# Performance work log

Hardware: AMD Instinct MI355X
Metric: run time of the kernel (lower is better)

## Reference

```python
import jax, jax.numpy as jnp
import numpy as np

PI_APPROX = 3.1415926  # the source uses 3.1415926, not math.pi
N_RINGS = 10
N_ANGLES = 36  # k in range(0, 360, 10)


def setup_inputs() -> dict:
    key = jax.random.key(0)
    k1, k2, k3 = jax.random.split(key, 3)
    B, N = 32, 16384
    pred = jax.random.normal(k1, (B, N_RINGS), dtype=jnp.float32)
    target = jax.random.normal(k2, (B, N, 3), dtype=jnp.float32)
    trans_feat = jax.random.normal(k3, (B, 256), dtype=jnp.float32)
    return {"pred": pred, "target": target, "trans_feat": trans_feat}


def _generate_points(pred):
    # pred: [B, 10] radii. For ring j: center = [0.04, 0.15*j - 0.7, 0.0],
    # axis = y, firstPoint (centered) = [-r, 0, 0]. Rotating about y by angle a:
    # R @ [-r,0,0] = [-r*cos(a), 0, r*sin(a)]; then add center back.
    B = pred.shape[0]
    j = jnp.arange(N_RINGS, dtype=pred.dtype)
    cy = 0.15 * j - 0.7                                   # [10]
    ang = jnp.arange(0, 360, 10, dtype=pred.dtype) * (2.0 * PI_APPROX / 360.0)  # [36]
    c, s = jnp.cos(ang), jnp.sin(ang)
    r = pred[:, :, None]                                  # [B,10,1]
    px = -r * c[None, None, :] + 0.04                     # [B,10,36]
    py = jnp.broadcast_to(cy[None, :, None], px.shape)    # [B,10,36]
    pz = r * s[None, None, :]                             # [B,10,36]
    pts = jnp.stack([px, py, pz], axis=-1)                # [B,10,36,3]
    return pts.reshape(B, N_RINGS * N_ANGLES, 3)          # [B,360,3]


def reference(pred, target, trans_feat):
    B = pred.shape[0]
    pts = _generate_points(pred.reshape(B, N_RINGS))      # [B,360,3]
    # squared pairwise distances via ||a||^2 + ||b||^2 - 2 a.b
    d2 = (jnp.sum(pts * pts, axis=-1)[:, :, None]
          + jnp.sum(target * target, axis=-1)[:, None, :]
          - 2.0 * jnp.einsum('bpd,bnd->bpn', pts, target))  # [B,360,N]
    d2 = jnp.maximum(d2, 0.0)
    # original: min over target of ||pt - tgt||, then squared == min of squared dist
    min_d2 = jnp.min(d2, axis=-1)                         # [B,360]
    return jnp.mean(min_d2)
```

## Files before the change

### kernel.cpp

```cpp
#include <hip/hip_runtime.h>
#include <math.h>
#include <float.h>

#define N_RINGS  10
#define N_ANGLES 36
#define NP       (N_RINGS * N_ANGLES)
#define PI_APPROX 3.1415926f

#define BLOCK  256
#define WPB    4
#define CHUNK  512
#define NPAIR  (CHUNK / 2)
#define PPT    6

typedef float f2 __attribute__((ext_vector_type(2)));

__global__ __launch_bounds__(BLOCK, 4) void chamfer_minbuf(
    const float* __restrict__ pred,
    const float* __restrict__ target,
    unsigned int* __restrict__ minbuf,
    int N, int chunks)
{
    __shared__ float4 txy[NPAIR];
    __shared__ float4 tzw[NPAIR];
    __shared__ float  pm[WPB * NP];
    __shared__ float  cs_c[N_ANGLES], cs_s[N_ANGLES];

    const int b   = blockIdx.x / chunks;
    const int cg  = blockIdx.x % chunks;
    const int n0  = cg * CHUNK;
    const int tid = threadIdx.x;
    const int cnt = min(CHUNK, N - n0);
    const int npairs = (cnt + 1) >> 1;

    if (tid < N_ANGLES) {
        float angf = (float)(10 * tid) * (2.0f * PI_APPROX / 360.0f);
        double ang = (double)angf;
        cs_c[tid] = (float)cos(ang);
        cs_s[tid] = (float)sin(ang);
    }
    for (int p = tid; p < npairs; p += BLOCK) {
        const int i0 = 2 * p;
        const int i1 = min(2 * p + 1, cnt - 1);
        const float* t0 = target + ((size_t)b * N + (size_t)(n0 + i0)) * 3;
        const float* t1 = target + ((size_t)b * N + (size_t)(n0 + i1)) * 3;
        float x0 = t0[0], y0 = t0[1], z0 = t0[2];
        float x1 = t1[0], y1 = t1[1], z1 = t1[2];
        float w0 = x0 * x0 + y0 * y0 + z0 * z0;
        float w1 = x1 * x1 + y1 * y1 + z1 * z1;
        txy[p] = make_float4(x0, x1, y0, y1);
        tzw[p] = make_float4(z0, z1, w0, w1);
    }
    __syncthreads();

    const int lane = tid & 63;
    const int w    = tid >> 6;

    f2 qx2[PPT], qy2[PPT], qz2[PPT];
    float m[PPT], pp2[PPT];
    #pragma unroll
    for (int k = 0; k < PPT; ++k) {
        int s = lane + 64 * k;
        int j = s / N_ANGLES;
        int a = s - j * N_ANGLES;
        int jc = (j < N_RINGS) ? j : (N_RINGS - 1);
        float r  = pred[b * N_RINGS + jc];
        float px = -r * cs_c[a] + 0.04f;
        float py = 0.15f * (float)jc - 0.7f;
        float pz = r * cs_s[a];
        pp2[k] = px * px + py * py + pz * pz;
        float qxv = -2.0f * px, qyv = -2.0f * py, qzv = -2.0f * pz;
        qx2[k] = (f2){qxv, qxv};
        qy2[k] = (f2){qyv, qyv};
        qz2[k] = (f2){qzv, qzv};
        m[k]   = FLT_MAX;
    }

    #pragma unroll 4
    for (int k = w; k < npairs; k += WPB) {
        float4 A  = txy[k];
        float4 Bz = tzw[k];
        f2 X  = {A.x,  A.y };
        f2 Y  = {A.z,  A.w };
        f2 Z  = {Bz.x, Bz.y};
        f2 W2 = {Bz.z, Bz.w};
        #pragma unroll
        for (int i = 0; i < PPT; ++i) {
            f2 h = __builtin_elementwise_fma(qz2[i], Z, W2);
            h = __builtin_elementwise_fma(qy2[i], Y, h);
            h = __builtin_elementwise_fma(qx2[i], X, h);
            m[i] = fminf(fminf(m[i], h.x), h.y);
        }
    }

    #pragma unroll
    for (int k = 0; k < PPT; ++k) {
        int s = lane + 64 * k;
        if (s < NP) pm[w * NP + s] = fmaxf(pp2[k] + m[k], 0.0f);
    }
    __syncthreads();

    for (int p = tid; p < NP; p += BLOCK) {
        float v = fminf(fminf(pm[p], pm[NP + p]),
                        fminf(pm[2 * NP + p], pm[3 * NP + p]));
        atomicMin(&minbuf[b * NP + p], __float_as_uint(v));
    }
}

__global__ __launch_bounds__(1024) void reduce_mean(
    const unsigned int* __restrict__ minbuf, float* __restrict__ out,
    int count)
{
    __shared__ double sm[16];
    const int tid = threadIdx.x;
    double s = 0.0;
    const int n4 = count >> 2;
    const uint4* v4 = (const uint4*)minbuf;
    for (int i = tid; i < n4; i += 1024) {
        uint4 u = v4[i];
        s += (double)__uint_as_float(u.x) + (double)__uint_as_float(u.y)
           + (double)__uint_as_float(u.z) + (double)__uint_as_float(u.w);
    }
    for (int i = 4 * n4 + tid; i < count; i += 1024)
        s += (double)__uint_as_float(minbuf[i]);
    #pragma unroll
    for (int off = 32; off > 0; off >>= 1)
        s += __shfl_down(s, off, 64);
    if ((tid & 63) == 0) sm[tid >> 6] = s;
    __syncthreads();
    if (tid == 0) {
        double tot = 0.0;
        for (int wv = 0; wv < 16; ++wv) tot += sm[wv];
        out[0] = (float)(tot / (double)count);
    }
}

extern "C" void kernel_launch(void* const* d_in, const int* in_sizes, int n_in,
                              void* d_out, int out_size, void* d_ws, size_t ws_size,
                              hipStream_t stream) {
    const float* pred   = (const float*)d_in[0];
    const float* target = (const float*)d_in[1];

    const int B = in_sizes[0] / N_RINGS;
    const int N = in_sizes[1] / (3 * B);
    const int chunks = (N + CHUNK - 1) / CHUNK;
    const int count  = B * NP;

    unsigned int* minbuf = (unsigned int*)d_ws;
    float* out = (float*)d_out;

    hipMemsetAsync(minbuf, 0xFF, (size_t)count * sizeof(unsigned int), stream);

    hipLaunchKernelGGL(chamfer_minbuf, dim3(B * chunks), dim3(BLOCK), 0, stream,
                       pred, target, minbuf, N, chunks);
    hipLaunchKernelGGL(reduce_mean, dim3(1), dim3(1024), 0, stream,
                       minbuf, out, count);
}
```

Baseline: 81.48 us.

## Replace atomicMin and memset with per-chunk partials and multi-block reduction

The main kernel now writes per-chunk minimum values to a partial buffer instead of doing global atomicMin into a memset-initialized buffer. This removes the memset launch and the atomic contention. A new multi-block reduce kernel takes the min across chunks for each point, sums the results, and uses an atomic counter so the last block computes the final mean. The cost is a larger workspace (B*chunks*360 floats) and the reduction having to read all partials.

Result: slower. 91.19 us (+11.9%).

```diff
diff --git a/kernel.cpp b/kernel.cpp
--- a/kernel.cpp
+++ b/kernel.cpp
@@ -12,13 +12,15 @@
 #define CHUNK  512
 #define NPAIR  (CHUNK / 2)
 #define PPT    6
+#define RBLOCK 256
 
 typedef float f2 __attribute__((ext_vector_type(2)));
 
-__global__ __launch_bounds__(BLOCK, 4) void chamfer_minbuf(
+__global__ __launch_bounds__(BLOCK, 4) void chamfer_partial(
     const float* __restrict__ pred,
     const float* __restrict__ target,
-    unsigned int* __restrict__ minbuf,
+    float* __restrict__ partial,
+    unsigned int* __restrict__ counter,
     int N, int chunks)
 {
     __shared__ float4 txy[NPAIR];
@@ -32,6 +34,9 @@
     const int tid = threadIdx.x;
     const int cnt = min(CHUNK, N - n0);
     const int npairs = (cnt + 1) >> 1;
+
+    if (blockIdx.x == 0 && tid == 0)
+        *counter = 0u;
 
     if (tid < N_ANGLES) {
         float angf = (float)(10 * tid) * (2.0f * PI_APPROX / 360.0f);
@@ -100,38 +105,58 @@
     }
     __syncthreads();
 
+    float* dst = partial + ((size_t)b * chunks + cg) * NP;
     for (int p = tid; p < NP; p += BLOCK) {
         float v = fminf(fminf(pm[p], pm[NP + p]),
                         fminf(pm[2 * NP + p], pm[3 * NP + p]));
-        atomicMin(&minbuf[b * NP + p], __float_as_uint(v));
+        dst[p] = v;
     }
 }
 
-__global__ __launch_bounds__(1024) void reduce_mean(
-    const unsigned int* __restrict__ minbuf, float* __restrict__ out,
-    int count)
+__global__ __launch_bounds__(RBLOCK) void reduce_minmean(
+    const float* __restrict__ partial,
+    double* __restrict__ sums,
+    unsigned int* __restrict__ counter,
+    float* __restrict__ out,
+    int chunks, int count, int nblocks)
 {
-    __shared__ double sm[16];
+    __shared__ double sm[RBLOCK / 64];
     const int tid = threadIdx.x;
+    const int gid = blockIdx.x * RBLOCK + tid;
+    const int lane = tid & 63;
+    const int w    = tid >> 6;
+
     double s = 0.0;
-    const int n4 = count >> 2;
-    const uint4* v4 = (const uint4*)minbuf;
-    for (int i = tid; i < n4; i += 1024) {
-        uint4 u = v4[i];
-        s += (double)__uint_as_float(u.x) + (double)__uint_as_float(u.y)
-           + (double)__uint_as_float(u.z) + (double)__uint_as_float(u.w);
+    if (gid < count) {
+        const int b = gid / NP;
+        const int p = gid - b * NP;
+        const float* base = partial + (size_t)b * chunks * NP + p;
+        float mv = base[0];
+        for (int c = 1; c < chunks; ++c)
+            mv = fminf(mv, base[(size_t)c * NP]);
+        s = (double)mv;
     }
-    for (int i = 4 * n4 + tid; i < count; i += 1024)
-        s += (double)__uint_as_float(minbuf[i]);
     #pragma unroll
     for (int off = 32; off > 0; off >>= 1)
         s += __shfl_down(s, off, 64);
-    if ((tid & 63) == 0) sm[tid >> 6] = s;
+    if (lane == 0) sm[w] = s;
     __syncthreads();
+
     if (tid == 0) {
         double tot = 0.0;
-        for (int wv = 0; wv < 16; ++wv) tot += sm[wv];
-        out[0] = (float)(tot / (double)count);
+        #pragma unroll
+        for (int wv = 0; wv < RBLOCK / 64; ++wv) tot += sm[wv];
+        __hip_atomic_store(&sums[blockIdx.x], tot, __ATOMIC_RELAXED,
+                           __HIP_MEMORY_SCOPE_AGENT);
+        unsigned int t = __hip_atomic_fetch_add(counter, 1u, __ATOMIC_ACQ_REL,
+                                                __HIP_MEMORY_SCOPE_AGENT);
+        if (t == (unsigned int)(nblocks - 1)) {
+            double g = 0.0;
+            for (int bk = 0; bk < nblocks; ++bk)
+                g += __hip_atomic_load(&sums[bk], __ATOMIC_RELAXED,
+                                       __HIP_MEMORY_SCOPE_AGENT);
+            out[0] = (float)(g / (double)count);
+        }
     }
 }
 
@@ -143,16 +168,19 @@
 
     const int B = in_sizes[0] / N_RINGS;
     const int N = in_sizes[1] / (3 * B);
-    const int chunks = (N + CHUNK - 1) / CHUNK;
-    const int count  = B * NP;
+    const int chunks  = (N + CHUNK - 1) / CHUNK;
+    const int count   = B * NP;
+    const int nblocks = (count + RBLOCK - 1) / RBLOCK;
 
-    unsigned int* minbuf = (unsigned int*)d_ws;
-    float* out = (float*)d_out;
+    const size_t partial_elems = (size_t)B * chunks * NP;
+    float*        partial = (float*)d_ws;
+    double*       sums    = (double*)((char*)d_ws +
+                            ((partial_elems * sizeof(float) + 7) & ~(size_t)7));
+    unsigned int* counter = (unsigned int*)(sums + nblocks);
+    float*        out     = (float*)d_out;
 
-    hipMemsetAsync(minbuf, 0xFF, (size_t)count * sizeof(unsigned int), stream);
-
-    hipLaunchKernelGGL(chamfer_minbuf, dim3(B * chunks), dim3(BLOCK), 0, stream,
-                       pred, target, minbuf, N, chunks);
-    hipLaunchKernelGGL(reduce_mean, dim3(1), dim3(1024), 0, stream,
-                       minbuf, out, count);
+    hipLaunchKernelGGL(chamfer_partial, dim3(B * chunks), dim3(BLOCK), 0,
+                       stream, pred, target, partial, counter, N, chunks);
+    hipLaunchKernelGGL(reduce_minmean, dim3(nblocks), dim3(RBLOCK), 0, stream,
+                       partial, sums, counter, out, chunks, count, nblocks);
 }
```
